# Kernel tuning notes

Hardware: AMD Instinct MI355X
Metric: run time of the kernel (lower is better)

## Reference

```python
import jax, jax.numpy as jnp
import numpy as np

S, A = 8, 2
SA = S + A
N = 256


def setup_inputs() -> dict:
    key = jax.random.key(0)
    ks = jax.random.split(key, 8)
    mean_full = jax.random.normal(ks[0], (SA,), dtype=jnp.float32)
    C = jax.random.normal(ks[1], (SA, SA), dtype=jnp.float32)
    cov_full = (C @ C.T) / SA + 0.1 * jnp.eye(SA, dtype=jnp.float32)  # PSD input covariance
    dynamics_inputs = jax.random.normal(ks[2], (N, SA), dtype=jnp.float32)
    dynamics_outputs = jax.random.normal(ks[3], (N, S), dtype=jnp.float32)
    eq_coeff = 0.5 + 0.5 * jax.random.uniform(ks[4], (S,), dtype=jnp.float32)
    eq_scales = 0.5 + 0.5 * jax.random.uniform(ks[5], (S, SA), dtype=jnp.float32)
    eq_noise_coeff = 1e-2 + 1e-2 * jax.random.uniform(ks[6], (S,), dtype=jnp.float32)
    return {
        'mean_full': mean_full,
        'cov_full': cov_full,
        'dynamics_inputs': dynamics_inputs,
        'dynamics_outputs': dynamics_outputs,
        'eq_coeff': eq_coeff,
        'eq_scales': eq_scales,
        'eq_noise_coeff': eq_noise_coeff,
    }


def _eq_kernel_log(x, x_, eq_coeff, eq_scales):
    # x: [n, d], x_: [m, d] -> [S, n, m] log kernel
    diffs = x[:, None, :] - x_[None, :, :]
    quads = jnp.einsum('nmd,nmd,gd->gnm', diffs, diffs, 1.0 / eq_scales)
    return jnp.log(eq_coeff)[:, None, None] - 0.5 * quads


def reference(mean_full, cov_full, dynamics_inputs, dynamics_outputs,
              eq_coeff, eq_scales, eq_noise_coeff):
    s_dim = eq_coeff.shape[0]
    sa = mean_full.shape[0]
    n = dynamics_inputs.shape[0]
    dtype = mean_full.dtype
    mean_full = mean_full.reshape(1, sa)
    cov_full = cov_full.reshape(sa, sa)
    inv_scales = 1.0 / eq_scales  # [S, SA]
    eye_sa = jnp.eye(sa, dtype=dtype)

    # data covariance K + noise: [S, N, N]
    log_K = _eq_kernel_log(dynamics_inputs, dynamics_inputs, eq_coeff, eq_scales)
    data_cov = jnp.exp(log_K) + eq_noise_coeff[:, None, None] * eye_sa[None, :n, :n] if n == sa else jnp.exp(log_K) + eq_noise_coeff[:, None, None] * jnp.eye(n, dtype=dtype)[None]
    # beta: [S, N]
    beta = jnp.linalg.solve(data_cov, dynamics_outputs.T[:, :, None])[:, :, 0]

    # mean determinant coefficient: det(cov_full diag(1/scales_g) + I)^(-1/2)
    M = cov_full[None, :, :] * inv_scales[:, None, :] + eye_sa[None]  # [S, SA, SA]
    mean_det_coeff = eq_coeff * jnp.linalg.det(M) ** (-0.5)  # [S]

    cov_full_plus_scales = cov_full[None] + jax.vmap(jnp.diag)(eq_scales)  # [S, SA, SA]
    nu = dynamics_inputs - mean_full  # [N, SA]
    sol = jnp.linalg.solve(cov_full_plus_scales,
                           jnp.broadcast_to(nu.T[None], (s_dim, sa, n)))  # [S, SA, N]
    mean_quad = jnp.einsum('id,gdi->gi', nu, sol)
    mean_exp_quad = mean_det_coeff[:, None] * jnp.exp(-0.5 * mean_quad)  # [S, N]
    mean = jnp.einsum('gi,gi->g', beta, mean_exp_quad)  # [S]

    # R_ab = cov_full (inv_a + inv_b) + I: [S, S, SA, SA]
    cross = inv_scales[:, None, :] + inv_scales[None, :, :]  # [S, S, SA]
    R = cov_full[None, None, :, :] * cross[:, :, None, :] + eye_sa[None, None]
    _, log_R_det = jnp.linalg.slogdet(R)
    log_R_det_inv_sqrt = -0.5 * log_R_det  # [S, S]

    log_k_data_mu = _eq_kernel_log(mean_full, dynamics_inputs, eq_coeff, eq_scales)  # [S, 1, N]
    log_k_ab = log_k_data_mu[None, :, :, :] + log_k_data_mu[:, :, :, None]  # [S, S, N, N]

    eq_scale_times_nu = nu[None, :, :] * inv_scales[:, None, :]  # [S, N, SA]
    z = (eq_scale_times_nu[:, None, :, None, :] +
         eq_scale_times_nu[None, :, None, :, :])  # [S, S, N, N, SA]
    # R^{-1} cov_full, then quadratic form z^T (R^{-1} cov_full) z
    R_inv = jnp.linalg.inv(R)  # [S, S, SA, SA]
    M_ab = jnp.einsum('abij,jk->abik', R_inv, cov_full)  # [S, S, SA, SA]
    cov_quad = 0.5 * jnp.einsum('abnmi,abij,abnmj->abnm', z, M_ab, z)

    log_Q = log_k_ab + cov_quad + log_R_det_inv_sqrt[:, :, None, None]
    Q = jnp.exp(log_Q)  # [S, S, N, N]

    Q_diag = Q[jnp.arange(s_dim), jnp.arange(s_dim)]  # [S, N, N]
    expected_var = eq_coeff - jnp.trace(jnp.linalg.solve(data_cov, Q_diag),
                                        axis1=-2, axis2=-1)  # [S]

    cov = jnp.einsum('ai,bj,abij->ab', beta, beta, Q)
    cov = cov - mean[:, None] * mean[None, :]
    cov = cov + jnp.diag(expected_var)

    # input-output cross covariance
    A_inv_mean = jnp.linalg.solve(cov_full_plus_scales,
                                  jnp.broadcast_to(mean_full.T[None], (s_dim, sa, 1)))  # [S, SA, 1]
    A_inv_dyn = jnp.linalg.solve(cov_full_plus_scales,
                                 jnp.broadcast_to(dynamics_inputs.T[None], (s_dim, sa, n)))  # [S, SA, N]
    cross_cov_mu = eq_scales[:, :, None] * A_inv_mean + jnp.einsum('ij,gjk->gik', cov_full, A_inv_dyn)
    cross_cov = jnp.einsum('gk,gdk,gk->dg', mean_exp_quad, cross_cov_mu, beta)  # [SA, S]
    cross_cov_s = cross_cov[:s_dim, :] - mean_full[:, :s_dim].T * mean[None, :]

    mean = mean + mean_full[0, :s_dim]
    cov = cov + cov_full[:s_dim, :s_dim]
    cov = cov + cross_cov_s + cross_cov_s.T
    return mean, cov
```

## Files before the change

kernel.cpp:

```cpp
#include <hip/hip_runtime.h>
#include <math.h>

#define S_DIM 8
#define SA_DIM 10
#define NN 256

constexpr size_t OFF_K     = 0;
constexpr size_t OFF_LINV  = OFF_K    + 8ull*NN*NN;
constexpr size_t OFF_KINV  = OFF_LINV + 8ull*NN*NN;
constexpr size_t OFF_RD    = OFF_KINV + 8ull*NN*NN;
constexpr size_t OFF_U     = OFF_RD   + 8*NN;
constexpr size_t OFF_LK    = OFF_U    + 8*NN*SA_DIM;
constexpr size_t OFF_M     = OFF_LK   + 8*NN;
constexpr size_t OFF_C     = OFF_M    + 64*100;
constexpr size_t OFF_AINV  = OFF_C    + 64;
constexpr size_t OFF_AIM   = OFF_AINV + 800;
constexpr size_t OFF_MDC   = OFF_AIM  + 80;
constexpr size_t OFF_BETA  = OFF_MDC  + 8;
constexpr size_t OFF_MEAN  = OFF_BETA + 8*NN;
constexpr size_t OFF_CROSS = OFF_MEAN + 8;
constexpr size_t OFF_COVP  = OFF_CROSS+ 80;
constexpr size_t OFF_TRP   = OFF_COVP + 256;

__device__ void gj_invert10(float A[SA_DIM][SA_DIM], float B[SA_DIM][SA_DIM], float* logdet) {
#pragma unroll
  for (int i = 0; i < SA_DIM; i++)
#pragma unroll
    for (int j = 0; j < SA_DIM; j++) B[i][j] = (i == j) ? 1.f : 0.f;
  float ld = 0.f;
#pragma unroll
  for (int k = 0; k < SA_DIM; k++) {
    float pv = A[k][k];
    ld += logf(pv);
    float ip = 1.f / pv;
#pragma unroll
    for (int j = 0; j < SA_DIM; j++) { A[k][j] *= ip; B[k][j] *= ip; }
#pragma unroll
    for (int r = 0; r < SA_DIM; r++) {
      if (r == k) continue;
      float f = A[r][k];
#pragma unroll
      for (int j = 0; j < SA_DIM; j++) { A[r][j] -= f * A[k][j]; B[r][j] -= f * B[k][j]; }
    }
  }
  *logdet = ld;
}

__global__ __launch_bounds__(256) void k_front(const float* __restrict__ x,
                                               const float* __restrict__ mf,
                                               const float* __restrict__ cov,
                                               const float* __restrict__ eqc,
                                               const float* __restrict__ scales,
                                               const float* __restrict__ noise,
                                               float* __restrict__ Kw,
                                               float* __restrict__ u,
                                               float* __restrict__ lkw,
                                               float* __restrict__ Mw, float* __restrict__ cvec,
                                               float* __restrict__ Ainvw, float* __restrict__ aimw,
                                               float* __restrict__ mdcw) {
  int blk = blockIdx.x;
  if (blk < 2048) {
    int g = blk >> 8;
    int n = blk & 255;
    int m = threadIdx.x;
    __shared__ float xs[NN * SA_DIM];
    __shared__ float isc[SA_DIM];
    for (int i = threadIdx.x; i < NN * SA_DIM; i += 256) xs[i] = x[i];
    if (threadIdx.x < SA_DIM) isc[threadIdx.x] = 1.0f / scales[g * SA_DIM + threadIdx.x];
    __syncthreads();
    float quad = 0.f;
#pragma unroll
    for (int d = 0; d < SA_DIM; d++) {
      float df = xs[n * SA_DIM + d] - xs[m * SA_DIM + d];
      quad += df * df * isc[d];
    }
    float v = eqc[g] * __expf(-0.5f * quad);
    if (m == n) v += noise[g];
    Kw[(size_t)g * NN * NN + (size_t)n * NN + m] = v;
  } else if (blk < 2056) {
    int g = blk - 2048;
    int n = threadIdx.x;
    float quad = 0.f;
#pragma unroll
    for (int d = 0; d < SA_DIM; d++) {
      float isc = 1.0f / scales[g * SA_DIM + d];
      float nu = x[n * SA_DIM + d] - mf[d];
      u[((size_t)g * NN + n) * SA_DIM + d] = nu * isc;
      quad += nu * nu * isc;
    }
    lkw[g * NN + n] = logf(eqc[g]) - 0.5f * quad;
  } else {
    int p = threadIdx.x;
    if (p >= 64) return;
    int a = p >> 3, b = p & 7;
    float A[SA_DIM][SA_DIM], B[SA_DIM][SA_DIM];
    for (int i = 0; i < SA_DIM; i++)
      for (int j = 0; j < SA_DIM; j++)
        A[i][j] = cov[i * SA_DIM + j] * (1.f / scales[a * SA_DIM + j] + 1.f / scales[b * SA_DIM + j]) +
                  ((i == j) ? 1.f : 0.f);
    float ld;
    gj_invert10(A, B, &ld);
    cvec[p] = -0.5f * ld;
    for (int i = 0; i < SA_DIM; i++)
      for (int j = 0; j < SA_DIM; j++) {
        float v = 0.f;
        for (int k = 0; k < SA_DIM; k++) v += B[i][k] * cov[k * SA_DIM + j];
        Mw[p * 100 + i * SA_DIM + j] = v;
      }
    if (b == 0) {
      int g = a;
      for (int i = 0; i < SA_DIM; i++)
        for (int j = 0; j < SA_DIM; j++)
          A[i][j] = cov[i * SA_DIM + j] + ((i == j) ? scales[g * SA_DIM + j] : 0.f);
      float ld2;
      gj_invert10(A, B, &ld2);
      for (int i = 0; i < SA_DIM; i++)
        for (int j = 0; j < SA_DIM; j++) Ainvw[g * 100 + i * SA_DIM + j] = B[i][j];
      for (int i = 0; i < SA_DIM; i++) {
        float v = 0.f;
        for (int j = 0; j < SA_DIM; j++) v += B[i][j] * mf[j];
        aimw[g * SA_DIM + i] = v;
      }
      for (int i = 0; i < SA_DIM; i++)
        for (int j = 0; j < SA_DIM; j++)
          A[i][j] = cov[i * SA_DIM + j] * (1.f / scales[g * SA_DIM + j]) + ((i == j) ? 1.f : 0.f);
      float ld3;
      gj_invert10(A, B, &ld3);
      mdcw[g] = eqc[g] * __expf(-0.5f * ld3);
    }
  }
}

__device__ __forceinline__ void tile_idx(int tau, int ntile, int nt4, int c0,
                                         int& ib, int& jb, int& iq, int& jq) {
  int rt = ntile - 1 - tau;
  int q = (int)((sqrtf((float)(8 * rt + 1)) - 1.0f) * 0.5f);
  while ((q + 1) * (q + 2) / 2 <= rt) q++;
  while (q * (q + 1) / 2 > rt) q--;
  jq = nt4 - 1 - q;
  int rem = rt - q * (q + 1) / 2;
  iq = nt4 - 1 - rem;
  jb = c0 + 16 + 4 * jq;
  ib = c0 + 16 + 4 * iq;
}

__device__ __forceinline__ void chol_factor_panel(float* __restrict__ Ag,
                                                  float* __restrict__ rdg,
                                                  int c0, int nb, int t, int lane,
                                                  bool fromGlobal,
                                                  const float (*SRC)[248],
                                                  float (*Pdst)[248]) {
  int rr = lane & 15;
  float a[16];
  float myrs = 0.f;
  if (fromGlobal) {
#pragma unroll
    for (int j = 0; j < 16; j++)
      a[j] = (j <= rr) ? Ag[(size_t)(c0 + j) * NN + (c0 + rr)]
                       : Ag[(size_t)(c0 + rr) * NN + (c0 + j)];
  } else {
#pragma unroll
    for (int j = 0; j < 16; j++)
      a[j] = (j <= rr) ? SRC[j][rr] : SRC[rr][j];
  }
#pragma unroll
  for (int k = 0; k < 16; k++) {
    float d = __shfl(a[k], k);
    float rs_ = rsqrtf(d);
    if (rr == k) myrs = rs_;
    float m = a[k] * rs_;
#pragma unroll
    for (int j = 0; j < 16; j++) {
      if (j > k) {
        float Lkj = __shfl(a[j], k) * rs_;
        a[j] = fmaf(-m, Lkj, a[j]);
      }
    }
    a[k] = m;
  }
  if (t < 16) {
    rdg[c0 + rr] = myrs;
#pragma unroll
    for (int j = 0; j < 16; j++)
      if (j <= rr) Ag[(size_t)(c0 + j) * NN + (c0 + rr)] = a[j];
  }
  if (t < nb) {
    int i = c0 + 16 + t;
    float xs[16];
#pragma unroll
    for (int c = 0; c < 16; c++) {
      float x = fromGlobal ? Ag[(size_t)(c0 + c) * NN + i] : SRC[c][16 + t];
#pragma unroll
      for (int cp = 0; cp < 16; cp++) {
        if (cp < c) {
          float Lccp = __shfl(a[cp], c);
          x = fmaf(-Lccp, xs[cp], x);
        }
      }
      xs[c] = x * __shfl(myrs, c);
    }
#pragma unroll
    for (int c = 0; c < 16; c++) {
      Ag[(size_t)(c0 + c) * NN + i] = xs[c];
      Pdst[c][t] = xs[c];
    }
  }
}

__global__ __launch_bounds__(1024, 4) void k_chol8(float* __restrict__ Aw,
                                                   float* __restrict__ rd) {
  int g = blockIdx.x;
  float* Ag = Aw + (size_t)g * NN * NN;
  float* rdg = rd + g * NN;
  int t = threadIdx.x;
  int lane = t & 63;
  int w = t >> 6;
  __shared__ __align__(16) float P[2][16][248];
  __shared__ __align__(16) float NP[16][248];

  if (w < 4)
    chol_factor_panel(Ag, rdg, 0, 240, t, lane, true, nullptr, P[0]);
  __syncthreads();

  for (int p = 0; p < 15; p++) {
    int c0 = 16 * p;
    int nb = NN - c0 - 16;
    int nt4 = nb >> 2;
    const float (*Pc)[248] = P[p & 1];
    int ncrit = 4 * nt4 - 6;
    if (t < ncrit) {
      int jq, iq;
      if (t < nt4) { jq = 0; iq = t; }
      else if (t < 2 * nt4 - 1) { jq = 1; iq = t - nt4 + 1; }
      else if (t < 3 * nt4 - 3) { jq = 2; iq = t - (2 * nt4 - 1) + 2; }
      else { jq = 3; iq = t - (3 * nt4 - 3) + 3; }
      int jb = c0 + 16 + 4 * jq, ib = c0 + 16 + 4 * iq;
      float4 cv0 = *(const float4*)(Ag + (size_t)(jb + 0) * NN + ib);
      float4 cv1 = *(const float4*)(Ag + (size_t)(jb + 1) * NN + ib);
      float4 cv2 = *(const float4*)(Ag + (size_t)(jb + 2) * NN + ib);
      float4 cv3 = *(const float4*)(Ag + (size_t)(jb + 3) * NN + ib);
      float4 a0 = make_float4(0.f, 0.f, 0.f, 0.f), a1 = a0, a2 = a0, a3 = a0;
#pragma unroll
      for (int k = 0; k < 16; k++) {
        float4 pi = *(const float4*)(&Pc[k][4 * iq]);
        float4 pj = *(const float4*)(&Pc[k][4 * jq]);
        a0.x = fmaf(pj.x, pi.x, a0.x); a0.y = fmaf(pj.x, pi.y, a0.y);
        a0.z = fmaf(pj.x, pi.z, a0.z); a0.w = fmaf(pj.x, pi.w, a0.w);
        a1.x = fmaf(pj.y, pi.x, a1.x); a1.y = fmaf(pj.y, pi.y, a1.y);
        a1.z = fmaf(pj.y, pi.z, a1.z); a1.w = fmaf(pj.y, pi.w, a1.w);
        a2.x = fmaf(pj.z, pi.x, a2.x); a2.y = fmaf(pj.z, pi.y, a2.y);
        a2.z = fmaf(pj.z, pi.z, a2.z); a2.w = fmaf(pj.z, pi.w, a2.w);
        a3.x = fmaf(pj.w, pi.x, a3.x); a3.y = fmaf(pj.w, pi.y, a3.y);
        a3.z = fmaf(pj.w, pi.z, a3.z); a3.w = fmaf(pj.w, pi.w, a3.w);
      }
      cv0.x -= a0.x; cv0.y -= a0.y; cv0.z -= a0.z; cv0.w -= a0.w;
      cv1.x -= a1.x; cv1.y -= a1.y; cv1.z -= a1.z; cv1.w -= a1.w;
      cv2.x -= a2.x; cv2.y -= a2.y; cv2.z -= a2.z; cv2.w -= a2.w;
      cv3.x -= a3.x; cv3.y -= a3.y; cv3.z -= a3.z; cv3.w -= a3.w;
      *(float4*)(&NP[4 * jq + 0][4 * iq]) = cv0;
      *(float4*)(&NP[4 * jq + 1][4 * iq]) = cv1;
      *(float4*)(&NP[4 * jq + 2][4 * iq]) = cv2;
      *(float4*)(&NP[4 * jq + 3][4 * iq]) = cv3;
    }
    __syncthreads();
    if (w < 4) {
      chol_factor_panel(Ag, rdg, c0 + 16, nb - 16, t, lane, false, NP, P[(p + 1) & 1]);
    } else {
      int nt4b = nt4 - 4;
      int ntileB = nt4b * (nt4b + 1) / 2;
      for (int tau = t - 256; tau < ntileB; tau += 768) {
        int ib, jb, iq, jq;
        tile_idx(tau, ntileB, nt4b, c0 + 16, ib, jb, iq, jq);
        float4 cv0 = *(const float4*)(Ag + (size_t)(jb + 0) * NN + ib);
        float4 cv1 = *(const float4*)(Ag + (size_t)(jb + 1) * NN + ib);
        float4 cv2 = *(const float4*)(Ag + (size_t)(jb + 2) * NN + ib);
        float4 cv3 = *(const float4*)(Ag + (size_t)(jb + 3) * NN + ib);
        float4 a0 = make_float4(0.f, 0.f, 0.f, 0.f), a1 = a0, a2 = a0, a3 = a0;
#pragma unroll
        for (int k = 0; k < 16; k++) {
          float4 pi = *(const float4*)(&Pc[k][16 + 4 * iq]);
          float4 pj = *(const float4*)(&Pc[k][16 + 4 * jq]);
          a0.x = fmaf(pj.x, pi.x, a0.x); a0.y = fmaf(pj.x, pi.y, a0.y);
          a0.z = fmaf(pj.x, pi.z, a0.z); a0.w = fmaf(pj.x, pi.w, a0.w);
          a1.x = fmaf(pj.y, pi.x, a1.x); a1.y = fmaf(pj.y, pi.y, a1.y);
          a1.z = fmaf(pj.y, pi.z, a1.z); a1.w = fmaf(pj.y, pi.w, a1.w);
          a2.x = fmaf(pj.z, pi.x, a2.x); a2.y = fmaf(pj.z, pi.y, a2.y);
          a2.z = fmaf(pj.z, pi.z, a2.z); a2.w = fmaf(pj.z, pi.w, a2.w);
          a3.x = fmaf(pj.w, pi.x, a3.x); a3.y = fmaf(pj.w, pi.y, a3.y);
          a3.z = fmaf(pj.w, pi.z, a3.z); a3.w = fmaf(pj.w, pi.w, a3.w);
        }
        cv0.x -= a0.x; cv0.y -= a0.y; cv0.z -= a0.z; cv0.w -= a0.w;
        cv1.x -= a1.x; cv1.y -= a1.y; cv1.z -= a1.z; cv1.w -= a1.w;
        cv2.x -= a2.x; cv2.y -= a2.y; cv2.z -= a2.z; cv2.w -= a2.w;
        cv3.x -= a3.x; cv3.y -= a3.y; cv3.z -= a3.z; cv3.w -= a3.w;
        *(float4*)(Ag + (size_t)(jb + 0) * NN + ib) = cv0;
        *(float4*)(Ag + (size_t)(jb + 1) * NN + ib) = cv1;
        *(float4*)(Ag + (size_t)(jb + 2) * NN + ib) = cv2;
        *(float4*)(Ag + (size_t)(jb + 3) * NN + ib) = cv3;
      }
    }
    __syncthreads();
  }
}

__global__ __launch_bounds__(256) void k_linv2(const float* __restrict__ LT,
                                               const float* __restrict__ rd,
                                               float* __restrict__ Linv) {
  int g = blockIdx.x >> 2;
  int q = blockIdx.x & 3;
  int w = threadIdx.x >> 6;
  int lane = threadIdx.x & 63;
  int j = 4 * q + w;
  const float* Ag = LT + (size_t)g * NN * NN;
  const float* rdg = rd + g * NN;
  float* Og = Linv + (size_t)g * NN * NN;
  __shared__ __align__(16) float Xl[4][16][16][16];
  __shared__ __align__(16) float Dv[16][16][16];
  int r = lane & 15, cq = lane >> 4;

  for (int s = 0; s < 4; s++) {
    int i = w + 4 * s;
    for (int e = lane; e < 256; e += 64) {
      int k = e >> 4, rr = e & 15;
      Xl[w][s][k][rr] = Ag[(size_t)(16 * i + k) * NN + 16 * i + rr];
    }
    asm volatile("s_waitcnt lgkmcnt(0)" ::: "memory");
    __builtin_amdgcn_sched_barrier(0);
    int c = lane & 15;
    float xv[16];
#pragma unroll
    for (int rr = 0; rr < 16; rr++) {
      float tmp = (rr == c) ? 1.f : 0.f;
#pragma unroll
      for (int m = 0; m < 16; m++) {
        if (m < rr) tmp = fmaf(-Xl[w][s][m][rr], xv[m], tmp);
      }
      xv[rr] = tmp * rdg[16 * i + rr];
    }
    if (lane < 16) {
#pragma unroll
      for (int rr = 0; rr < 16; rr++) Dv[i][rr][lane] = xv[rr];
    }
  }
  __syncthreads();

  {
    float4 dj = *(const float4*)&Dv[j][r][4 * cq];
    *(float4*)&Xl[w][j][r][4 * cq] = dj;
    *(float4*)(Og + (size_t)(16 * j + r) * NN + 16 * j + 4 * cq) = dj;
    float4 z = make_float4(0.f, 0.f, 0.f, 0.f);
    for (int i2 = 0; i2 < j; i2++)
      *(float4*)(Og + (size_t)(16 * i2 + r) * NN + 16 * j + 4 * cq) = z;
  }
  asm volatile("s_waitcnt lgkmcnt(0)" ::: "memory");
  __builtin_amdgcn_sched_barrier(0);

  for (int i = j + 1; i < 16; i++) {
    float4 acc = make_float4(0.f, 0.f, 0.f, 0.f);
    for (int k = j; k < i; k++) {
      const float* Lbase = Ag + (size_t)(16 * k) * NN + 16 * i + r;
      const float* Xk = &Xl[w][k][0][4 * cq];
#pragma unroll
      for (int m = 0; m < 16; m++) {
        float lv = Lbase[(size_t)m * NN];
        float4 xvv = *(const float4*)(Xk + 16 * m);
        acc.x = fmaf(lv, xvv.x, acc.x);
        acc.y = fmaf(lv, xvv.y, acc.y);
        acc.z = fmaf(lv, xvv.z, acc.z);
        acc.w = fmaf(lv, xvv.w, acc.w);
      }
    }
    float4 o = make_float4(0.f, 0.f, 0.f, 0.f);
#pragma unroll
    for (int m = 0; m < 16; m++) {
      float d = Dv[i][r][m];
      float sx = __shfl(acc.x, m + 16 * cq);
      float sy = __shfl(acc.y, m + 16 * cq);
      float sz = __shfl(acc.z, m + 16 * cq);
      float sw = __shfl(acc.w, m + 16 * cq);
      o.x = fmaf(-d, sx, o.x);
      o.y = fmaf(-d, sy, o.y);
      o.z = fmaf(-d, sz, o.z);
      o.w = fmaf(-d, sw, o.w);
    }
    *(float4*)&Xl[w][i][r][4 * cq] = o;
    *(float4*)(Og + (size_t)(16 * i + r) * NN + 16 * j + 4 * cq) = o;
    asm volatile("s_waitcnt lgkmcnt(0)" ::: "memory");
    __builtin_amdgcn_sched_barrier(0);
  }
}

__global__ __launch_bounds__(256) void k_syrk(const float* __restrict__ Linv,
                                              float* __restrict__ Kinv) {
  int g = blockIdx.x >> 4;
  int tile = blockIdx.x & 15;
  int i0 = (tile >> 2) * 64, j0 = (tile & 3) * 64;
  const float* A = Linv + (size_t)g * NN * NN;
  float* O = Kinv + (size_t)g * NN * NN;
  __shared__ float sa[32][64], sb[32][64];
  int tx = threadIdx.x & 15, ty = threadIdx.x >> 4;
  float acc[4][4] = {{0.f}};
  for (int k0 = 0; k0 < NN; k0 += 32) {
    for (int e = threadIdx.x; e < 2048; e += 256) {
      int kk = e >> 6, cc = e & 63;
      sa[kk][cc] = A[(size_t)(k0 + kk) * NN + i0 + cc];
      sb[kk][cc] = A[(size_t)(k0 + kk) * NN + j0 + cc];
    }
    __syncthreads();
#pragma unroll 8
    for (int kk = 0; kk < 32; kk++) {
      float av[4], bv[4];
#pragma unroll
      for (int q = 0; q < 4; q++) { av[q] = sa[kk][ty * 4 + q]; bv[q] = sb[kk][tx * 4 + q]; }
#pragma unroll
      for (int q = 0; q < 4; q++)
#pragma unroll
        for (int r = 0; r < 4; r++) acc[q][r] += av[q] * bv[r];
    }
    __syncthreads();
  }
#pragma unroll
  for (int q = 0; q < 4; q++)
#pragma unroll
    for (int r = 0; r < 4; r++)
      O[(size_t)(i0 + ty * 4 + q) * NN + j0 + tx * 4 + r] = acc[q][r];
}

__global__ __launch_bounds__(256) void k_beta(const float* __restrict__ Kinv,
                                              const float* __restrict__ y,
                                              float* __restrict__ betaw) {
  int g = blockIdx.x, n = threadIdx.x;
  __shared__ __align__(16) float ys[NN];
  ys[n] = y[n * S_DIM + g];
  __syncthreads();
  const float4* Kg = (const float4*)(Kinv + (size_t)g * NN * NN + (size_t)n * NN);
  float acc = 0.f;
  for (int m4 = 0; m4 < 64; m4++) {
    float4 kv = Kg[m4];
    float4 yv = ((const float4*)ys)[m4];
    acc += kv.x * yv.x + kv.y * yv.y + kv.z * yv.z + kv.w * yv.w;
  }
  betaw[g * NN + n] = acc;
}

__global__ __launch_bounds__(256) void k_back(const float* __restrict__ u,
                                              const float* __restrict__ lkw,
                                              const float* __restrict__ Mw,
                                              const float* __restrict__ cvec,
                                              const float* __restrict__ Kinv,
                                              const float* __restrict__ betaw,
                                              const float* __restrict__ x,
                                              const float* __restrict__ mf,
                                              const float* __restrict__ cov,
                                              const float* __restrict__ scales,
                                              const float* __restrict__ Ainvw,
                                              const float* __restrict__ aimw,
                                              const float* __restrict__ mdcw,
                                              float* __restrict__ covp, float* __restrict__ trp,
                                              float* __restrict__ meanw, float* __restrict__ crossw) {
  int blk = blockIdx.x;
  int t = threadIdx.x;
  if (blk < 256) {
    int p = blk >> 2;
    int quarter = blk & 3;
    int a = p >> 3, b = p & 7;
    __shared__ __align__(16) float ub[NN * 12];
    __shared__ float Ms[100];
    __shared__ float sbv[NN];
    __shared__ float eb[NN];
    __shared__ float red[256];
    {
      const float* ur = u + (size_t)b * NN * SA_DIM + (size_t)t * SA_DIM;
      float* ud = &ub[t * 12];
#pragma unroll
      for (int d = 0; d < SA_DIM; d++) ud[d] = ur[d];
    }
    if (t < 100) Ms[t] = Mw[p * 100 + t];
    eb[t] = betaw[b * NN + t];
    __syncthreads();
    {
      const float* um = &ub[t * 12];
      float qd = 0.f;
#pragma unroll
      for (int d = 0; d < SA_DIM; d++) {
        float v = 0.f;
#pragma unroll
        for (int e = 0; e < SA_DIM; e++) v += Ms[d * SA_DIM + e] * um[e];
        qd += v * um[d];
      }
      sbv[t] = lkw[b * NN + t] + 0.5f * qd;
    }
    __syncthreads();
    int n = quarter * 64 + (t >> 2);
    int c = t & 3;
    float ua[SA_DIM];
#pragma unroll
    for (int d = 0; d < SA_DIM; d++) ua[d] = u[((size_t)a * NN + n) * SA_DIM + d];
    float va[SA_DIM];
#pragma unroll
    for (int d = 0; d < SA_DIM; d++) {
      float v = 0.f;
#pragma unroll
      for (int e = 0; e < SA_DIM; e++) v += Ms[d * SA_DIM + e] * ua[e];
      va[d] = v;
    }
    float qa = 0.f;
#pragma unroll
    for (int d = 0; d < SA_DIM; d++) qa += va[d] * ua[d];
    float pa = lkw[a * NN + n] + 0.5f * qa + cvec[p];
    float wa = betaw[a * NN + n];
    const float* Krow = Kinv + (size_t)a * NN * NN + (size_t)n * NN;
    float covacc = 0.f, tracc = 0.f;
    bool dg = (a == b);
    for (int ii = 0; ii < 64; ii++) {
      int mm = c + 4 * ii;
      const float* ur = &ub[mm * 12];
      float4 f0 = *(const float4*)ur;
      float4 f1 = *(const float4*)(ur + 4);
      float4 f2 = *(const float4*)(ur + 8);
      float s = pa + sbv[mm];
      s += va[0] * f0.x + va[1] * f0.y + va[2] * f0.z + va[3] * f0.w;
      s += va[4] * f1.x + va[5] * f1.y + va[6] * f1.z + va[7] * f1.w;
      s += va[8] * f2.x + va[9] * f2.y;
      float e = __expf(s);
      covacc += eb[mm] * e;
      if (dg) tracc += Krow[mm] * e;
    }
    covacc *= wa;
    red[t] = covacc;
    __syncthreads();
    for (int st = 128; st > 0; st >>= 1) {
      if (t < st) red[t] += red[t + st];
      __syncthreads();
    }
    if (t == 0) covp[blk] = red[0];
    if (dg) {
      red[t] = tracc;
      __syncthreads();
      for (int st = 128; st > 0; st >>= 1) {
        if (t < st) red[t] += red[t + st];
        __syncthreads();
      }
      if (t == 0) trp[a * 4 + quarter] = red[0];
    }
  } else {
    int g = blk - 256;
    int i = t;
    __shared__ float Ai[100], cv[100], aims[SA_DIM], sc[SA_DIM], mfs[SA_DIM];
    __shared__ float red[256];
    if (i < 100) { Ai[i] = Ainvw[g * 100 + i]; cv[i] = cov[i]; }
    if (i < SA_DIM) { aims[i] = aimw[g * SA_DIM + i]; sc[i] = scales[g * SA_DIM + i]; mfs[i] = mf[i]; }
    __syncthreads();
    float bg = betaw[g * NN + i];
    float xi[SA_DIM], nu[SA_DIM];
#pragma unroll
    for (int d = 0; d < SA_DIM; d++) { xi[d] = x[i * SA_DIM + d]; nu[d] = xi[d] - mfs[d]; }
    float sv[SA_DIM], ad[SA_DIM];
#pragma unroll
    for (int d = 0; d < SA_DIM; d++) {
      float s1 = 0.f, s2 = 0.f;
#pragma unroll
      for (int e = 0; e < SA_DIM; e++) { s1 += Ai[d * SA_DIM + e] * nu[e]; s2 += Ai[d * SA_DIM + e] * xi[e]; }
      sv[d] = s1;
      ad[d] = s2;
    }
    float mq = 0.f;
#pragma unroll
    for (int d = 0; d < SA_DIM; d++) mq += nu[d] * sv[d];
    float mexp = mdcw[g] * __expf(-0.5f * mq);
    float cm = bg * mexp;
    float contrib[SA_DIM];
#pragma unroll
    for (int d = 0; d < SA_DIM; d++) {
      float ccm = sc[d] * aims[d];
#pragma unroll
      for (int jj = 0; jj < SA_DIM; jj++) ccm += cv[d * SA_DIM + jj] * ad[jj];
      contrib[d] = mexp * ccm * bg;
    }
    red[i] = cm;
    __syncthreads();
    for (int st = 128; st > 0; st >>= 1) {
      if (i < st) red[i] += red[i + st];
      __syncthreads();
    }
    if (i == 0) meanw[g] = red[0];
    for (int d = 0; d < SA_DIM; d++) {
      __syncthreads();
      red[i] = contrib[d];
      __syncthreads();
      for (int st = 128; st > 0; st >>= 1) {
        if (i < st) red[i] += red[i + st];
        __syncthreads();
      }
      if (i == 0) crossw[d * S_DIM + g] = red[0];
    }
  }
}

__global__ __launch_bounds__(64) void k_final(const float* __restrict__ covp,
                                              const float* __restrict__ trp,
                                              const float* __restrict__ meanw,
                                              const float* __restrict__ crossw,
                                              const float* __restrict__ cov,
                                              const float* __restrict__ eqc,
                                              const float* __restrict__ mf,
                                              float* __restrict__ out) {
  int p = threadIdx.x;
  if (p >= 64) return;
  int a = p >> 3, b = p & 7;
  float covq = covp[p * 4] + covp[p * 4 + 1] + covp[p * 4 + 2] + covp[p * 4 + 3];
  float ma = meanw[a], mb = meanw[b];
  float val = covq - ma * mb + cov[a * SA_DIM + b];
  if (a == b) {
    float tr = trp[a * 4] + trp[a * 4 + 1] + trp[a * 4 + 2] + trp[a * 4 + 3];
    val += eqc[a] - tr;
  }
  val += (crossw[a * S_DIM + b] - mf[a] * mb) + (crossw[b * S_DIM + a] - mf[b] * ma);
  out[S_DIM + p] = val;
  if (p < S_DIM) out[p] = meanw[p] + mf[p];
}

extern "C" void kernel_launch(void* const* d_in, const int* in_sizes, int n_in,
                              void* d_out, int out_size, void* d_ws, size_t ws_size,
                              hipStream_t stream) {
  const float* mf     = (const float*)d_in[0];
  const float* cov    = (const float*)d_in[1];
  const float* x      = (const float*)d_in[2];
  const float* y      = (const float*)d_in[3];
  const float* eqc    = (const float*)d_in[4];
  const float* scales = (const float*)d_in[5];
  const float* noise  = (const float*)d_in[6];
  float* ws = (float*)d_ws;

  float* Kw    = ws + OFF_K;
  float* Linv  = ws + OFF_LINV;
  float* Kinv  = ws + OFF_KINV;
  float* rd    = ws + OFF_RD;
  float* u     = ws + OFF_U;
  float* lkw   = ws + OFF_LK;
  float* Mw    = ws + OFF_M;
  float* cvec  = ws + OFF_C;
  float* Ainvw = ws + OFF_AINV;
  float* aimw  = ws + OFF_AIM;
  float* mdcw  = ws + OFF_MDC;
  float* betaw = ws + OFF_BETA;
  float* meanw = ws + OFF_MEAN;
  float* crossw= ws + OFF_CROSS;
  float* covp  = ws + OFF_COVP;
  float* trp   = ws + OFF_TRP;

  k_front<<<2057, 256, 0, stream>>>(x, mf, cov, eqc, scales, noise, Kw, u, lkw, Mw, cvec,
                                    Ainvw, aimw, mdcw);
  k_chol8<<<8, 1024, 0, stream>>>(Kw, rd);
  k_linv2<<<32, 256, 0, stream>>>(Kw, rd, Linv);
  k_syrk<<<128, 256, 0, stream>>>(Linv, Kinv);
  k_beta<<<8, 256, 0, stream>>>(Kinv, y, betaw);
  k_back<<<264, 256, 0, stream>>>(u, lkw, Mw, cvec, Kinv, betaw, x, mf, cov, scales,
                                  Ainvw, aimw, mdcw, covp, trp, meanw, crossw);
  k_final<<<1, 64, 0, stream>>>(covp, trp, meanw, crossw, cov, eqc, mf, (float*)d_out);
}
```

Baseline: 268.4 us.

## Keep entire upper-triangular matrix in LDS during blocked Cholesky

The Cholesky kernel now loads the whole upper triangle of each 256x256 matrix into a packed shared-memory array (about 130 KB), stored in 4-row blocks. The trailing updates and panel factorizations read and write LDS instead of global memory, and only the final factor rows are written back to global memory. The former P/NP panel staging buffers are removed. This is meant to remove repeated global-memory round trips in the serial 15-step loop. The large LDS footprint limits each CU to one block, but only 8 blocks are launched, and the packed layout may cause bank conflicts.

```diff
diff --git a/kernel.cpp b/kernel.cpp
--- a/kernel.cpp
+++ b/kernel.cpp
@@ -144,25 +144,25 @@
   ib = c0 + 16 + 4 * iq;
 }
 
-__device__ __forceinline__ void chol_factor_panel(float* __restrict__ Ag,
-                                                  float* __restrict__ rdg,
-                                                  int c0, int nb, int t, int lane,
-                                                  bool fromGlobal,
-                                                  const float (*SRC)[248],
-                                                  float (*Pdst)[248]) {
+__device__ __forceinline__ int tri_base(int j) {
+  int B = j >> 2, r = j & 3;
+  return 1024 * B - 8 * B * (B - 1) + r * (256 - 4 * B);
+}
+__device__ __forceinline__ float* tri_row(float* T, int j) {
+  return T + tri_base(j) - (j & ~3);
+}
+
+__device__ __forceinline__ void chol_factor_panel9(float* __restrict__ TRI,
+                                                   float* __restrict__ Ag,
+                                                   float* __restrict__ rdg,
+                                                   int c0, int nb, int t, int lane) {
   int rr = lane & 15;
   float a[16];
   float myrs = 0.f;
-  if (fromGlobal) {
-#pragma unroll
-    for (int j = 0; j < 16; j++)
-      a[j] = (j <= rr) ? Ag[(size_t)(c0 + j) * NN + (c0 + rr)]
-                       : Ag[(size_t)(c0 + rr) * NN + (c0 + j)];
-  } else {
-#pragma unroll
-    for (int j = 0; j < 16; j++)
-      a[j] = (j <= rr) ? SRC[j][rr] : SRC[rr][j];
-  }
+#pragma unroll
+  for (int j = 0; j < 16; j++)
+    a[j] = (j <= rr) ? tri_row(TRI, c0 + j)[c0 + rr]
+                     : tri_row(TRI, c0 + rr)[c0 + j];
 #pragma unroll
   for (int k = 0; k < 16; k++) {
     float d = __shfl(a[k], k);
@@ -182,14 +182,17 @@
     rdg[c0 + rr] = myrs;
 #pragma unroll
     for (int j = 0; j < 16; j++)
-      if (j <= rr) Ag[(size_t)(c0 + j) * NN + (c0 + rr)] = a[j];
+      if (j <= rr) {
+        Ag[(size_t)(c0 + j) * NN + (c0 + rr)] = a[j];
+        tri_row(TRI, c0 + j)[c0 + rr] = a[j];
+      }
   }
   if (t < nb) {
     int i = c0 + 16 + t;
     float xs[16];
 #pragma unroll
     for (int c = 0; c < 16; c++) {
-      float x = fromGlobal ? Ag[(size_t)(c0 + c) * NN + i] : SRC[c][16 + t];
+      float x = tri_row(TRI, c0 + c)[i];
 #pragma unroll
       for (int cp = 0; cp < 16; cp++) {
         if (cp < c) {
@@ -202,31 +205,39 @@
 #pragma unroll
     for (int c = 0; c < 16; c++) {
       Ag[(size_t)(c0 + c) * NN + i] = xs[c];
-      Pdst[c][t] = xs[c];
-    }
-  }
-}
-
-__global__ __launch_bounds__(1024, 4) void k_chol8(float* __restrict__ Aw,
-                                                   float* __restrict__ rd) {
+      tri_row(TRI, c0 + c)[i] = xs[c];
+    }
+  }
+}
+
+__global__ __launch_bounds__(1024) void k_chol9(float* __restrict__ Aw,
+                                                float* __restrict__ rd) {
   int g = blockIdx.x;
   float* Ag = Aw + (size_t)g * NN * NN;
   float* rdg = rd + g * NN;
   int t = threadIdx.x;
   int lane = t & 63;
   int w = t >> 6;
-  __shared__ __align__(16) float P[2][16][248];
-  __shared__ __align__(16) float NP[16][248];
+  __shared__ __align__(16) float TRI[33280];
+
+  for (int j = w; j < NN; j += 16) {
+    int cnt = 64 - (j >> 2);
+    if (lane < cnt) {
+      int c = (j & ~3) + 4 * lane;
+      float4 v = *(const float4*)(Ag + (size_t)j * NN + c);
+      *(float4*)(tri_row(TRI, j) + c) = v;
+    }
+  }
+  __syncthreads();
 
   if (w < 4)
-    chol_factor_panel(Ag, rdg, 0, 240, t, lane, true, nullptr, P[0]);
+    chol_factor_panel9(TRI, Ag, rdg, 0, 240, t, lane);
   __syncthreads();
 
   for (int p = 0; p < 15; p++) {
     int c0 = 16 * p;
     int nb = NN - c0 - 16;
     int nt4 = nb >> 2;
-    const float (*Pc)[248] = P[p & 1];
     int ncrit = 4 * nt4 - 6;
     if (t < ncrit) {
       int jq, iq;
@@ -235,15 +246,16 @@
       else if (t < 3 * nt4 - 3) { jq = 2; iq = t - (2 * nt4 - 1) + 2; }
       else { jq = 3; iq = t - (3 * nt4 - 3) + 3; }
       int jb = c0 + 16 + 4 * jq, ib = c0 + 16 + 4 * iq;
-      float4 cv0 = *(const float4*)(Ag + (size_t)(jb + 0) * NN + ib);
-      float4 cv1 = *(const float4*)(Ag + (size_t)(jb + 1) * NN + ib);
-      float4 cv2 = *(const float4*)(Ag + (size_t)(jb + 2) * NN + ib);
-      float4 cv3 = *(const float4*)(Ag + (size_t)(jb + 3) * NN + ib);
+      float4 cv0 = *(const float4*)(tri_row(TRI, jb + 0) + ib);
+      float4 cv1 = *(const float4*)(tri_row(TRI, jb + 1) + ib);
+      float4 cv2 = *(const float4*)(tri_row(TRI, jb + 2) + ib);
+      float4 cv3 = *(const float4*)(tri_row(TRI, jb + 3) + ib);
       float4 a0 = make_float4(0.f, 0.f, 0.f, 0.f), a1 = a0, a2 = a0, a3 = a0;
 #pragma unroll
       for (int k = 0; k < 16; k++) {
-        float4 pi = *(const float4*)(&Pc[k][4 * iq]);
-        float4 pj = *(const float4*)(&Pc[k][4 * jq]);
+        const float* Lk = tri_row(TRI, c0 + k);
+        float4 pi = *(const float4*)(Lk + ib);
+        float4 pj = *(const float4*)(Lk + jb);
         a0.x = fmaf(pj.x, pi.x, a0.x); a0.y = fmaf(pj.x, pi.y, a0.y);
         a0.z = fmaf(pj.x, pi.z, a0.z); a0.w = fmaf(pj.x, pi.w, a0.w);
         a1.x = fmaf(pj.y, pi.x, a1.x); a1.y = fmaf(pj.y, pi.y, a1.y);
@@ -257,29 +269,30 @@
       cv1.x -= a1.x; cv1.y -= a1.y; cv1.z -= a1.z; cv1.w -= a1.w;
       cv2.x -= a2.x; cv2.y -= a2.y; cv2.z -= a2.z; cv2.w -= a2.w;
       cv3.x -= a3.x; cv3.y -= a3.y; cv3.z -= a3.z; cv3.w -= a3.w;
-      *(float4*)(&NP[4 * jq + 0][4 * iq]) = cv0;
-      *(float4*)(&NP[4 * jq + 1][4 * iq]) = cv1;
-      *(float4*)(&NP[4 * jq + 2][4 * iq]) = cv2;
-      *(float4*)(&NP[4 * jq + 3][4 * iq]) = cv3;
+      *(float4*)(tri_row(TRI, jb + 0) + ib) = cv0;
+      *(float4*)(tri_row(TRI, jb + 1) + ib) = cv1;
+      *(float4*)(tri_row(TRI, jb + 2) + ib) = cv2;
+      *(float4*)(tri_row(TRI, jb + 3) + ib) = cv3;
     }
     __syncthreads();
     if (w < 4) {
-      chol_factor_panel(Ag, rdg, c0 + 16, nb - 16, t, lane, false, NP, P[(p + 1) & 1]);
+      chol_factor_panel9(TRI, Ag, rdg, c0 + 16, nb - 16, t, lane);
     } else {
       int nt4b = nt4 - 4;
       int ntileB = nt4b * (nt4b + 1) / 2;
       for (int tau = t - 256; tau < ntileB; tau += 768) {
         int ib, jb, iq, jq;
         tile_idx(tau, ntileB, nt4b, c0 + 16, ib, jb, iq, jq);
-        float4 cv0 = *(const float4*)(Ag + (size_t)(jb + 0) * NN + ib);
-        float4 cv1 = *(const float4*)(Ag + (size_t)(jb + 1) * NN + ib);
-        float4 cv2 = *(const float4*)(Ag + (size_t)(jb + 2) * NN + ib);
-        float4 cv3 = *(const float4*)(Ag + (size_t)(jb + 3) * NN + ib);
+        float4 cv0 = *(const float4*)(tri_row(TRI, jb + 0) + ib);
+        float4 cv1 = *(const float4*)(tri_row(TRI, jb + 1) + ib);
+        float4 cv2 = *(const float4*)(tri_row(TRI, jb + 2) + ib);
+        float4 cv3 = *(const float4*)(tri_row(TRI, jb + 3) + ib);
         float4 a0 = make_float4(0.f, 0.f, 0.f, 0.f), a1 = a0, a2 = a0, a3 = a0;
 #pragma unroll
         for (int k = 0; k < 16; k++) {
-          float4 pi = *(const float4*)(&Pc[k][16 + 4 * iq]);
-          float4 pj = *(const float4*)(&Pc[k][16 + 4 * jq]);
+          const float* Lk = tri_row(TRI, c0 + k);
+          float4 pi = *(const float4*)(Lk + ib);
+          float4 pj = *(const float4*)(Lk + jb);
           a0.x = fmaf(pj.x, pi.x, a0.x); a0.y = fmaf(pj.x, pi.y, a0.y);
           a0.z = fmaf(pj.x, pi.z, a0.z); a0.w = fmaf(pj.x, pi.w, a0.w);
           a1.x = fmaf(pj.y, pi.x, a1.x); a1.y = fmaf(pj.y, pi.y, a1.y);
@@ -293,10 +306,10 @@
         cv1.x -= a1.x; cv1.y -= a1.y; cv1.z -= a1.z; cv1.w -= a1.w;
         cv2.x -= a2.x; cv2.y -= a2.y; cv2.z -= a2.z; cv2.w -= a2.w;
         cv3.x -= a3.x; cv3.y -= a3.y; cv3.z -= a3.z; cv3.w -= a3.w;
-        *(float4*)(Ag + (size_t)(jb + 0) * NN + ib) = cv0;
-        *(float4*)(Ag + (size_t)(jb + 1) * NN + ib) = cv1;
-        *(float4*)(Ag + (size_t)(jb + 2) * NN + ib) = cv2;
-        *(float4*)(Ag + (size_t)(jb + 3) * NN + ib) = cv3;
+        *(float4*)(tri_row(TRI, jb + 0) + ib) = cv0;
+        *(float4*)(tri_row(TRI, jb + 1) + ib) = cv1;
+        *(float4*)(tri_row(TRI, jb + 2) + ib) = cv2;
+        *(float4*)(tri_row(TRI, jb + 3) + ib) = cv3;
       }
     }
     __syncthreads();
@@ -651,7 +664,7 @@
 
   k_front<<<2057, 256, 0, stream>>>(x, mf, cov, eqc, scales, noise, Kw, u, lkw, Mw, cvec,
                                     Ainvw, aimw, mdcw);
-  k_chol8<<<8, 1024, 0, stream>>>(Kw, rd);
+  k_chol9<<<8, 1024, 0, stream>>>(Kw, rd);
   k_linv2<<<32, 256, 0, stream>>>(Kw, rd, Linv);
   k_syrk<<<128, 256, 0, stream>>>(Linv, Kinv);
   k_beta<<<8, 256, 0, stream>>>(Kinv, y, betaw);
```

Result: slower. 285.9 us (+6.5%).

## Use 8x8 register tiles in Cholesky trailing update and split k_back finer

Applied to the files above, without the earlier changes.

The Cholesky trailing-update phase now gives each thread an 8x8 tile instead of a 4x4 tile. This raises FMA work per shared-memory load and cuts the number of tile-index computations, at the cost of more registers per thread (64 accumulators). Separately, the k_back covariance/trace phase is split into eighths instead of quarters, doubling the grid to spread the N loop over more blocks. The final reduction and workspace offsets are updated to match.

```diff
diff --git a/kernel.cpp b/kernel.cpp
--- a/kernel.cpp
+++ b/kernel.cpp
@@ -20,7 +20,7 @@
 constexpr size_t OFF_MEAN  = OFF_BETA + 8*NN;
 constexpr size_t OFF_CROSS = OFF_MEAN + 8;
 constexpr size_t OFF_COVP  = OFF_CROSS+ 80;
-constexpr size_t OFF_TRP   = OFF_COVP + 256;
+constexpr size_t OFF_TRP   = OFF_COVP + 512;
 
 __device__ void gj_invert10(float A[SA_DIM][SA_DIM], float B[SA_DIM][SA_DIM], float* logdet) {
 #pragma unroll
@@ -131,19 +131,6 @@
   }
 }
 
-__device__ __forceinline__ void tile_idx(int tau, int ntile, int nt4, int c0,
-                                         int& ib, int& jb, int& iq, int& jq) {
-  int rt = ntile - 1 - tau;
-  int q = (int)((sqrtf((float)(8 * rt + 1)) - 1.0f) * 0.5f);
-  while ((q + 1) * (q + 2) / 2 <= rt) q++;
-  while (q * (q + 1) / 2 > rt) q--;
-  jq = nt4 - 1 - q;
-  int rem = rt - q * (q + 1) / 2;
-  iq = nt4 - 1 - rem;
-  jb = c0 + 16 + 4 * jq;
-  ib = c0 + 16 + 4 * iq;
-}
-
 __device__ __forceinline__ void chol_factor_panel(float* __restrict__ Ag,
                                                   float* __restrict__ rdg,
                                                   int c0, int nb, int t, int lane,
@@ -207,8 +194,8 @@
   }
 }
 
-__global__ __launch_bounds__(1024, 4) void k_chol8(float* __restrict__ Aw,
-                                                   float* __restrict__ rd) {
+__global__ __launch_bounds__(1024, 4) void k_chol12(float* __restrict__ Aw,
+                                                    float* __restrict__ rd) {
   int g = blockIdx.x;
   float* Ag = Aw + (size_t)g * NN * NN;
   float* rdg = rd + g * NN;
@@ -266,37 +253,56 @@
     if (w < 4) {
       chol_factor_panel(Ag, rdg, c0 + 16, nb - 16, t, lane, false, NP, P[(p + 1) & 1]);
     } else {
-      int nt4b = nt4 - 4;
-      int ntileB = nt4b * (nt4b + 1) / 2;
-      for (int tau = t - 256; tau < ntileB; tau += 768) {
-        int ib, jb, iq, jq;
-        tile_idx(tau, ntileB, nt4b, c0 + 16, ib, jb, iq, jq);
-        float4 cv0 = *(const float4*)(Ag + (size_t)(jb + 0) * NN + ib);
-        float4 cv1 = *(const float4*)(Ag + (size_t)(jb + 1) * NN + ib);
-        float4 cv2 = *(const float4*)(Ag + (size_t)(jb + 2) * NN + ib);
-        float4 cv3 = *(const float4*)(Ag + (size_t)(jb + 3) * NN + ib);
-        float4 a0 = make_float4(0.f, 0.f, 0.f, 0.f), a1 = a0, a2 = a0, a3 = a0;
-#pragma unroll
-        for (int k = 0; k < 16; k++) {
-          float4 pi = *(const float4*)(&Pc[k][16 + 4 * iq]);
-          float4 pj = *(const float4*)(&Pc[k][16 + 4 * jq]);
-          a0.x = fmaf(pj.x, pi.x, a0.x); a0.y = fmaf(pj.x, pi.y, a0.y);
-          a0.z = fmaf(pj.x, pi.z, a0.z); a0.w = fmaf(pj.x, pi.w, a0.w);
-          a1.x = fmaf(pj.y, pi.x, a1.x); a1.y = fmaf(pj.y, pi.y, a1.y);
-          a1.z = fmaf(pj.y, pi.z, a1.z); a1.w = fmaf(pj.y, pi.w, a1.w);
-          a2.x = fmaf(pj.z, pi.x, a2.x); a2.y = fmaf(pj.z, pi.y, a2.y);
-          a2.z = fmaf(pj.z, pi.z, a2.z); a2.w = fmaf(pj.z, pi.w, a2.w);
-          a3.x = fmaf(pj.w, pi.x, a3.x); a3.y = fmaf(pj.w, pi.y, a3.y);
-          a3.z = fmaf(pj.w, pi.z, a3.z); a3.w = fmaf(pj.w, pi.w, a3.w);
+      int m8 = (NN - c0 - 32) >> 3;
+      if (m8 > 0) {
+        int T8 = m8 * (m8 + 1) / 2;
+        for (int tau = t - 256; tau < T8; tau += 768) {
+          int rt = T8 - 1 - tau;
+          int q = (int)((sqrtf((float)(8 * rt + 1)) - 1.0f) * 0.5f);
+          while ((q + 1) * (q + 2) / 2 <= rt) q++;
+          while (q * (q + 1) / 2 > rt) q--;
+          int J = m8 - 1 - q;
+          int rem = rt - q * (q + 1) / 2;
+          int I = m8 - 1 - rem;
+          int jb = c0 + 32 + 8 * J;
+          int ib = c0 + 32 + 8 * I;
+          int pio = 16 + 8 * I;
+          int pjo = 16 + 8 * J;
+          float4 acc[16];
+#pragma unroll
+          for (int e = 0; e < 16; e++) acc[e] = make_float4(0.f, 0.f, 0.f, 0.f);
+#pragma unroll
+          for (int k = 0; k < 16; k++) {
+            float4 pi0 = *(const float4*)(&Pc[k][pio]);
+            float4 pi1 = *(const float4*)(&Pc[k][pio + 4]);
+            float4 pj0 = *(const float4*)(&Pc[k][pjo]);
+            float4 pj1 = *(const float4*)(&Pc[k][pjo + 4]);
+#define BUPD(jj, sv)                                                  \
+            acc[2*(jj)+0].x = fmaf((sv), pi0.x, acc[2*(jj)+0].x);     \
+            acc[2*(jj)+0].y = fmaf((sv), pi0.y, acc[2*(jj)+0].y);     \
+            acc[2*(jj)+0].z = fmaf((sv), pi0.z, acc[2*(jj)+0].z);     \
+            acc[2*(jj)+0].w = fmaf((sv), pi0.w, acc[2*(jj)+0].w);     \
+            acc[2*(jj)+1].x = fmaf((sv), pi1.x, acc[2*(jj)+1].x);     \
+            acc[2*(jj)+1].y = fmaf((sv), pi1.y, acc[2*(jj)+1].y);     \
+            acc[2*(jj)+1].z = fmaf((sv), pi1.z, acc[2*(jj)+1].z);     \
+            acc[2*(jj)+1].w = fmaf((sv), pi1.w, acc[2*(jj)+1].w);
+            BUPD(0, pj0.x) BUPD(1, pj0.y) BUPD(2, pj0.z) BUPD(3, pj0.w)
+            BUPD(4, pj1.x) BUPD(5, pj1.y) BUPD(6, pj1.z) BUPD(7, pj1.w)
+#undef BUPD
+          }
+#pragma unroll
+          for (int jj = 0; jj < 8; jj++) {
+            float* row = Ag + (size_t)(jb + jj) * NN + ib;
+            float4 c0v = *(const float4*)(row);
+            float4 c1v = *(const float4*)(row + 4);
+            c0v.x -= acc[2 * jj].x; c0v.y -= acc[2 * jj].y;
+            c0v.z -= acc[2 * jj].z; c0v.w -= acc[2 * jj].w;
+            c1v.x -= acc[2 * jj + 1].x; c1v.y -= acc[2 * jj + 1].y;
+            c1v.z -= acc[2 * jj + 1].z; c1v.w -= acc[2 * jj + 1].w;
+            *(float4*)(row) = c0v;
+            *(float4*)(row + 4) = c1v;
+          }
         }
-        cv0.x -= a0.x; cv0.y -= a0.y; cv0.z -= a0.z; cv0.w -= a0.w;
-        cv1.x -= a1.x; cv1.y -= a1.y; cv1.z -= a1.z; cv1.w -= a1.w;
-        cv2.x -= a2.x; cv2.y -= a2.y; cv2.z -= a2.z; cv2.w -= a2.w;
-        cv3.x -= a3.x; cv3.y -= a3.y; cv3.z -= a3.z; cv3.w -= a3.w;
-        *(float4*)(Ag + (size_t)(jb + 0) * NN + ib) = cv0;
-        *(float4*)(Ag + (size_t)(jb + 1) * NN + ib) = cv1;
-        *(float4*)(Ag + (size_t)(jb + 2) * NN + ib) = cv2;
-        *(float4*)(Ag + (size_t)(jb + 3) * NN + ib) = cv3;
       }
     }
     __syncthreads();
@@ -460,9 +466,9 @@
                                               float* __restrict__ meanw, float* __restrict__ crossw) {
   int blk = blockIdx.x;
   int t = threadIdx.x;
-  if (blk < 256) {
-    int p = blk >> 2;
-    int quarter = blk & 3;
+  if (blk < 512) {
+    int p = blk >> 3;
+    int eighth = blk & 7;
     int a = p >> 3, b = p & 7;
     __shared__ __align__(16) float ub[NN * 12];
     __shared__ float Ms[100];
@@ -491,8 +497,8 @@
       sbv[t] = lkw[b * NN + t] + 0.5f * qd;
     }
     __syncthreads();
-    int n = quarter * 64 + (t >> 2);
-    int c = t & 3;
+    int n = eighth * 32 + (t >> 3);
+    int c = t & 7;
     float ua[SA_DIM];
 #pragma unroll
     for (int d = 0; d < SA_DIM; d++) ua[d] = u[((size_t)a * NN + n) * SA_DIM + d];
@@ -512,8 +518,8 @@
     const float* Krow = Kinv + (size_t)a * NN * NN + (size_t)n * NN;
     float covacc = 0.f, tracc = 0.f;
     bool dg = (a == b);
-    for (int ii = 0; ii < 64; ii++) {
-      int mm = c + 4 * ii;
+    for (int ii = 0; ii < 32; ii++) {
+      int mm = c + 8 * ii;
       const float* ur = &ub[mm * 12];
       float4 f0 = *(const float4*)ur;
       float4 f1 = *(const float4*)(ur + 4);
@@ -541,10 +547,10 @@
         if (t < st) red[t] += red[t + st];
         __syncthreads();
       }
-      if (t == 0) trp[a * 4 + quarter] = red[0];
+      if (t == 0) trp[a * 8 + eighth] = red[0];
     }
   } else {
-    int g = blk - 256;
+    int g = blk - 512;
     int i = t;
     __shared__ float Ai[100], cv[100], aims[SA_DIM], sc[SA_DIM], mfs[SA_DIM];
     __shared__ float red[256];
@@ -608,11 +614,15 @@
   int p = threadIdx.x;
   if (p >= 64) return;
   int a = p >> 3, b = p & 7;
-  float covq = covp[p * 4] + covp[p * 4 + 1] + covp[p * 4 + 2] + covp[p * 4 + 3];
+  float covq = 0.f;
+#pragma unroll
+  for (int e = 0; e < 8; e++) covq += covp[p * 8 + e];
   float ma = meanw[a], mb = meanw[b];
   float val = covq - ma * mb + cov[a * SA_DIM + b];
   if (a == b) {
-    float tr = trp[a * 4] + trp[a * 4 + 1] + trp[a * 4 + 2] + trp[a * 4 + 3];
+    float tr = 0.f;
+#pragma unroll
+    for (int e = 0; e < 8; e++) tr += trp[a * 8 + e];
     val += eqc[a] - tr;
   }
   val += (crossw[a * S_DIM + b] - mf[a] * mb) + (crossw[b * S_DIM + a] - mf[b] * ma);
@@ -651,11 +661,11 @@
 
   k_front<<<2057, 256, 0, stream>>>(x, mf, cov, eqc, scales, noise, Kw, u, lkw, Mw, cvec,
                                     Ainvw, aimw, mdcw);
-  k_chol8<<<8, 1024, 0, stream>>>(Kw, rd);
+  k_chol12<<<8, 1024, 0, stream>>>(Kw, rd);
   k_linv2<<<32, 256, 0, stream>>>(Kw, rd, Linv);
   k_syrk<<<128, 256, 0, stream>>>(Linv, Kinv);
   k_beta<<<8, 256, 0, stream>>>(Kinv, y, betaw);
-  k_back<<<264, 256, 0, stream>>>(u, lkw, Mw, cvec, Kinv, betaw, x, mf, cov, scales,
+  k_back<<<520, 256, 0, stream>>>(u, lkw, Mw, cvec, Kinv, betaw, x, mf, cov, scales,
                                   Ainvw, aimw, mdcw, covp, trp, meanw, crossw);
   k_final<<<1, 64, 0, stream>>>(covp, trp, meanw, crossw, cov, eqc, mf, (float*)d_out);
 }
```

After: 339.7 us. 1.27x slower.
